# Kernel optimization log

Measured on AMD Instinct MI355X. Metric: run time of the kernel, lower is better.

Reference implementation:

```python
import jax, jax.numpy as jnp
import numpy as np

EPS = 1e-12


def _cosine_cost_volume(ref, tgt, D):
    """PSMNet-style shifted cosine-correlation cost volume, num_groups=1.
    ref, tgt: [B, C, Hf, Wf] quarter-res features. Returns [B, 1, D, Hf, Wf];
    positions w < d are 0 (zero-padded target -> zero cosine)."""
    B, C, Hf, Wf = ref.shape
    rn = ref * jax.lax.rsqrt(jnp.sum(ref * ref, axis=1, keepdims=True) + EPS)
    tn = tgt * jax.lax.rsqrt(jnp.sum(tgt * tgt, axis=1, keepdims=True) + EPS)
    pad = jnp.pad(tn, ((0, 0), (0, 0), (0, 0), (D - 1, 0)))  # left zero-pad

    def one_disp(d):
        t = jax.lax.dynamic_slice_in_dim(pad, D - 1 - d, Wf, axis=3)
        return jnp.sum(rn * t, axis=1)  # [B, Hf, Wf]

    vol = jax.vmap(one_disp)(jnp.arange(D))  # [D, B, Hf, Wf]
    return jnp.transpose(vol, (1, 0, 2, 3))[:, None]  # [B, 1, D, Hf, Wf]


def setup_inputs() -> dict:
    key = jax.random.key(0)
    k1, k2 = jax.random.split(key)
    B, C, Hf, Wf = 1, 32, 96, 192  # quarter-res ViT features (out_feats=32)
    left_fea = jax.random.normal(k1, (B, C, Hf, Wf), dtype=jnp.float32)
    right_fea = jax.random.normal(k2, (B, C, Hf, Wf), dtype=jnp.float32)
    return {"left_fea": left_fea, "right_fea": right_fea, "H": 384, "W": 768, "maxdisp": 192}


def reference(left_fea, right_fea, H, W, maxdisp):
    B = left_fea.shape[0]
    # training-branch cost volume (W//4 disparity levels, not detached in source)
    cost_init = _cosine_cost_volume(left_fea, right_fea, W // 4)
    # inference path: maxdisp//4 levels, trilinear upsample to [maxdisp, H, W]
    cost = _cosine_cost_volume(left_fea, right_fea, maxdisp // 4)
    cost = jax.lax.stop_gradient(cost)
    cost_up = jax.image.resize(cost, (B, 1, maxdisp, H, W), method="trilinear")
    pred = jnp.argmax(cost_up, axis=2)  # [B, 1, H, W]
    pred = jnp.maximum(pred, 1).astype(jnp.float32)  # pred[pred<1]=1
    return cost_init, pred
```

## Files before the change

### kernel.cpp

```cpp
#include <hip/hip_runtime.h>
#include <math.h>

#define HF 96
#define WF 192
#define CC 32
#define NPIX (HF*WF)
#define DFULL 192
#define DQ 48
#define HO 384
#define WO 768
#define SR 200

__global__ __launch_bounds__(256) void kcost(const float* __restrict__ L,
                                             const float* __restrict__ R,
                                             float* __restrict__ out) {
    __shared__ __align__(16) float Ls[CC * WF];
    __shared__ __align__(16) float Rb[CC * SR];
    const int h = blockIdx.x;
    const int tid = threadIdx.x;

    for (int i = tid; i < CC * 4; i += 256) Rb[(i >> 2) * SR + (i & 3)] = 0.0f;

    if (tid < WF) {
        const int w = tid;
        float lr[CC], rr[CC];
        float sl = 0.0f, sr = 0.0f;
        #pragma unroll
        for (int c = 0; c < CC; ++c) {
            float lv = L[c * NPIX + h * WF + w];
            float rv = R[c * NPIX + h * WF + w];
            lr[c] = lv; rr[c] = rv;
            sl = fmaf(lv, lv, sl);
            sr = fmaf(rv, rv, sr);
        }
        const float il = 1.0f / sqrtf(sl + 1e-12f);
        const float ir = 1.0f / sqrtf(sr + 1e-12f);
        #pragma unroll
        for (int c = 0; c < CC; ++c) {
            Ls[c * WF + w] = lr[c] * il;
            Rb[c * SR + 4 + w] = rr[c] * ir;
        }
    }
    __syncthreads();

    const int t = blockIdx.y * 256 + tid;
    if (t >= 1176) return;

    const int u = 1175 - t;
    int wu = (int)((sqrtf(8.0f * (float)u + 1.0f) - 1.0f) * 0.5f);
    while ((wu + 1) * (wu + 2) / 2 <= u) ++wu;
    while (wu * (wu + 1) / 2 > u) --wu;
    const int du = u - wu * (wu + 1) / 2;
    const int wt = 47 - du;
    const int dt = 47 - wu;

    const int w0 = wt * 4, d0 = dt * 4;
    const int base = w0 - d0;

    float a00=0,a01=0,a02=0,a03=0;
    float a10=0,a11=0,a12=0,a13=0;
    float a20=0,a21=0,a22=0,a23=0;
    float a30=0,a31=0,a32=0,a33=0;

    #pragma unroll 4
    for (int c = 0; c < CC; ++c) {
        const float4 lv = *(const float4*)&Ls[c * WF + w0];
        const float4 r0 = *(const float4*)&Rb[c * SR + base];
        const float4 r1 = *(const float4*)&Rb[c * SR + base + 4];
        a00 = fmaf(lv.x, r1.x, a00); a01 = fmaf(lv.y, r1.y, a01);
        a02 = fmaf(lv.z, r1.z, a02); a03 = fmaf(lv.w, r1.w, a03);
        a10 = fmaf(lv.x, r0.w, a10); a11 = fmaf(lv.y, r1.x, a11);
        a12 = fmaf(lv.z, r1.y, a12); a13 = fmaf(lv.w, r1.z, a13);
        a20 = fmaf(lv.x, r0.z, a20); a21 = fmaf(lv.y, r0.w, a21);
        a22 = fmaf(lv.z, r1.x, a22); a23 = fmaf(lv.w, r1.y, a23);
        a30 = fmaf(lv.x, r0.y, a30); a31 = fmaf(lv.y, r0.z, a31);
        a32 = fmaf(lv.z, r0.w, a32); a33 = fmaf(lv.w, r1.x, a33);
    }

    {
        float4 v;
        v.x=a00; v.y=a01; v.z=a02; v.w=a03;
        *(float4*)&out[(d0 + 0) * NPIX + h * WF + w0] = v;
        v.x=a10; v.y=a11; v.z=a12; v.w=a13;
        *(float4*)&out[(d0 + 1) * NPIX + h * WF + w0] = v;
        v.x=a20; v.y=a21; v.z=a22; v.w=a23;
        *(float4*)&out[(d0 + 2) * NPIX + h * WF + w0] = v;
        v.x=a30; v.y=a31; v.z=a32; v.w=a33;
        *(float4*)&out[(d0 + 3) * NPIX + h * WF + w0] = v;
    }

    if (wt > dt) {
        const int za = (wt - dt - 1) * 4;
        const int zb = (47 - dt) * 4;
        const float4 z = {0.0f, 0.0f, 0.0f, 0.0f};
        #pragma unroll
        for (int j = 0; j < 4; ++j)
            *(float4*)&out[(zb + j) * NPIX + h * WF + za] = z;
    }
}

__global__ __launch_bounds__(256) void kpred(const float* __restrict__ cost,
                                             float* __restrict__ pred) {
    const int mIdx = blockIdx.x * 64 + threadIdx.x;
    const int h = blockIdx.y * 4 + threadIdx.y;
    if (mIdx > 192) return;
    const int m = mIdx - 1;

    float sh = (float)(2 * h - 3) * 0.125f;
    float fh = sh - floorf(sh);
    int h0 = (int)floorf(sh);
    int h1 = h0 + 1;
    if (h0 < 0)      { h0 = 0; h1 = 0; fh = 0.0f; }
    if (h1 > HF - 1) { h1 = HF - 1;    fh = 0.0f; }
    const float wh0 = 1.0f - fh, wh1 = fh;

    const bool edge = (m < 0) || (m >= WF - 1);
    const int w0 = (m < 0) ? 0 : ((m >= WF - 1) ? WF - 1 : m);
    const int w1 = (m < 0) ? 0 : ((m >= WF - 1) ? WF - 1 : m + 1);

    float fr[4];
    #pragma unroll
    for (int r = 0; r < 4; ++r) fr[r] = edge ? 0.0f : (0.125f + 0.25f * (float)r);

    const int i00 = h0 * WF + w0;
    const int i10 = h1 * WF + w0;
    const int i01 = h0 * WF + w1;
    const int i11 = h1 * WF + w1;

    float bp[4], best[4];
    int bi[4];
    {
        const float* s = cost;
        float q00 = s[i00], q10 = s[i10], q01 = s[i01], q11 = s[i11];
        float A0 = fmaf(wh1, q10, wh0 * q00);
        float A1 = fmaf(wh1, q11, wh0 * q01);
        #pragma unroll
        for (int r = 0; r < 4; ++r) {
            bp[r] = fmaf(fr[r], A1, (1.0f - fr[r]) * A0);
            best[r] = bp[r];
            bi[r] = 0;
        }
    }

    for (int k = 1; k < DQ; ++k) {
        const float* s = cost + k * NPIX;
        float q00 = s[i00], q10 = s[i10], q01 = s[i01], q11 = s[i11];
        float A0 = fmaf(wh1, q10, wh0 * q00);
        float A1 = fmaf(wh1, q11, wh0 * q01);
        #pragma unroll
        for (int r = 0; r < 4; ++r) {
            float b = fmaf(fr[r], A1, (1.0f - fr[r]) * A0);
            float cand; int ci;
            if (b > bp[r]) { cand = fmaf(0.875f, b, 0.125f * bp[r]); ci = 4 * k + 1; }
            else           { cand = fmaf(0.125f, b, 0.875f * bp[r]); ci = 4 * k - 2; }
            if (cand > best[r]) { best[r] = cand; bi[r] = ci; }
            bp[r] = b;
        }
    }
    #pragma unroll
    for (int r = 0; r < 4; ++r)
        if (bp[r] > best[r]) bi[r] = 190;

    float v[4];
    #pragma unroll
    for (int r = 0; r < 4; ++r) v[r] = (float)(bi[r] < 1 ? 1 : bi[r]);

    float* prow = pred + h * WO;
    if (m < 0) {
        float2 o; o.x = v[0]; o.y = v[0];
        *(float2*)&prow[0] = o;
    } else if (m >= WF - 1) {
        float2 o; o.x = v[0]; o.y = v[0];
        *(float2*)&prow[WO - 2] = o;
    } else {
        float2 o0; o0.x = v[0]; o0.y = v[1];
        float2 o1; o1.x = v[2]; o1.y = v[3];
        *(float2*)&prow[4 * m + 2] = o0;
        *(float2*)&prow[4 * m + 4] = o1;
    }
}

extern "C" void kernel_launch(void* const* d_in, const int* in_sizes, int n_in,
                              void* d_out, int out_size, void* d_ws, size_t ws_size,
                              hipStream_t stream) {
    const float* L = (const float*)d_in[0];
    const float* R = (const float*)d_in[1];
    float* out = (float*)d_out;
    float* pred = out + DFULL * NPIX;

    kcost<<<dim3(HF, 5), 256, 0, stream>>>(L, R, out);
    kpred<<<dim3(4, HF), dim3(64, 4), 0, stream>>>(out, pred);
}
```

Before: 99.02 us.

## Use 4x8 register tiles and direct grid mapping in cost-volume kernel

Each thread of the cost-volume kernel now computes a 4-wide by 8-disparity tile instead of 4x4, and the triangular index decoding with sqrt and fix-up loops is replaced by a plain row-major tile index. Tiles that lie entirely in the w<d region simply write zeros and exit. Blocks shrink to 192 threads on a 96x6 grid, and the shared right-feature buffer gets an 8-element zero pad. The larger tile reuses each left-feature shared-memory load across more FMAs, at the cost of more registers and some idle threads on zero tiles.

```diff
diff --git a/kernel.cpp b/kernel.cpp
--- a/kernel.cpp
+++ b/kernel.cpp
@@ -9,19 +9,19 @@
 #define DQ 48
 #define HO 384
 #define WO 768
-#define SR 200
+#define SR2 200
 
-__global__ __launch_bounds__(256) void kcost(const float* __restrict__ L,
+__global__ __launch_bounds__(192) void kcost(const float* __restrict__ L,
                                              const float* __restrict__ R,
                                              float* __restrict__ out) {
     __shared__ __align__(16) float Ls[CC * WF];
-    __shared__ __align__(16) float Rb[CC * SR];
+    __shared__ __align__(16) float Rb[CC * SR2];
     const int h = blockIdx.x;
     const int tid = threadIdx.x;
 
-    for (int i = tid; i < CC * 4; i += 256) Rb[(i >> 2) * SR + (i & 3)] = 0.0f;
+    for (int i = tid; i < CC * 8; i += 192) Rb[(i >> 3) * SR2 + (i & 7)] = 0.0f;
 
-    if (tid < WF) {
+    {
         const int w = tid;
         float lr[CC], rr[CC];
         float sl = 0.0f, sr = 0.0f;
@@ -38,64 +38,54 @@
         #pragma unroll
         for (int c = 0; c < CC; ++c) {
             Ls[c * WF + w] = lr[c] * il;
-            Rb[c * SR + 4 + w] = rr[c] * ir;
+            Rb[c * SR2 + 8 + w] = rr[c] * ir;
         }
     }
     __syncthreads();
 
-    const int t = blockIdx.y * 256 + tid;
-    if (t >= 1176) return;
+    const int t = blockIdx.y * 192 + tid;
+    const int dt = t / 48;
+    const int wt = t - dt * 48;
+    const int w0 = wt * 4, d0 = dt * 8;
 
-    const int u = 1175 - t;
-    int wu = (int)((sqrtf(8.0f * (float)u + 1.0f) - 1.0f) * 0.5f);
-    while ((wu + 1) * (wu + 2) / 2 <= u) ++wu;
-    while (wu * (wu + 1) / 2 > u) --wu;
-    const int du = u - wu * (wu + 1) / 2;
-    const int wt = 47 - du;
-    const int dt = 47 - wu;
+    if (wt < 2 * dt) {
+        const float4 z = {0.0f, 0.0f, 0.0f, 0.0f};
+        #pragma unroll
+        for (int j = 0; j < 8; ++j)
+            *(float4*)&out[(d0 + j) * NPIX + h * WF + w0] = z;
+        return;
+    }
 
-    const int w0 = wt * 4, d0 = dt * 4;
     const int base = w0 - d0;
 
-    float a00=0,a01=0,a02=0,a03=0;
-    float a10=0,a11=0,a12=0,a13=0;
-    float a20=0,a21=0,a22=0,a23=0;
-    float a30=0,a31=0,a32=0,a33=0;
+    float acc[8][4];
+    #pragma unroll
+    for (int j = 0; j < 8; ++j)
+        #pragma unroll
+        for (int i = 0; i < 4; ++i) acc[j][i] = 0.0f;
 
     #pragma unroll 4
     for (int c = 0; c < CC; ++c) {
-        const float4 lv = *(const float4*)&Ls[c * WF + w0];
-        const float4 r0 = *(const float4*)&Rb[c * SR + base];
-        const float4 r1 = *(const float4*)&Rb[c * SR + base + 4];
-        a00 = fmaf(lv.x, r1.x, a00); a01 = fmaf(lv.y, r1.y, a01);
-        a02 = fmaf(lv.z, r1.z, a02); a03 = fmaf(lv.w, r1.w, a03);
-        a10 = fmaf(lv.x, r0.w, a10); a11 = fmaf(lv.y, r1.x, a11);
-        a12 = fmaf(lv.z, r1.y, a12); a13 = fmaf(lv.w, r1.z, a13);
-        a20 = fmaf(lv.x, r0.z, a20); a21 = fmaf(lv.y, r0.w, a21);
-        a22 = fmaf(lv.z, r1.x, a22); a23 = fmaf(lv.w, r1.y, a23);
-        a30 = fmaf(lv.x, r0.y, a30); a31 = fmaf(lv.y, r0.z, a31);
-        a32 = fmaf(lv.z, r0.w, a32); a33 = fmaf(lv.w, r1.x, a33);
+        const float4 lq = *(const float4*)&Ls[c * WF + w0];
+        const float lv[4] = {lq.x, lq.y, lq.z, lq.w};
+        float rr[12];
+        const float4 ra = *(const float4*)&Rb[c * SR2 + base];
+        const float4 rb = *(const float4*)&Rb[c * SR2 + base + 4];
+        const float4 rc = *(const float4*)&Rb[c * SR2 + base + 8];
+        rr[0]=ra.x; rr[1]=ra.y; rr[2]=ra.z; rr[3]=ra.w;
+        rr[4]=rb.x; rr[5]=rb.y; rr[6]=rb.z; rr[7]=rb.w;
+        rr[8]=rc.x; rr[9]=rc.y; rr[10]=rc.z; rr[11]=rc.w;
+        #pragma unroll
+        for (int j = 0; j < 8; ++j)
+            #pragma unroll
+            for (int i = 0; i < 4; ++i)
+                acc[j][i] = fmaf(lv[i], rr[8 + i - j], acc[j][i]);
     }
 
-    {
-        float4 v;
-        v.x=a00; v.y=a01; v.z=a02; v.w=a03;
-        *(float4*)&out[(d0 + 0) * NPIX + h * WF + w0] = v;
-        v.x=a10; v.y=a11; v.z=a12; v.w=a13;
-        *(float4*)&out[(d0 + 1) * NPIX + h * WF + w0] = v;
-        v.x=a20; v.y=a21; v.z=a22; v.w=a23;
-        *(float4*)&out[(d0 + 2) * NPIX + h * WF + w0] = v;
-        v.x=a30; v.y=a31; v.z=a32; v.w=a33;
-        *(float4*)&out[(d0 + 3) * NPIX + h * WF + w0] = v;
-    }
-
-    if (wt > dt) {
-        const int za = (wt - dt - 1) * 4;
-        const int zb = (47 - dt) * 4;
-        const float4 z = {0.0f, 0.0f, 0.0f, 0.0f};
-        #pragma unroll
-        for (int j = 0; j < 4; ++j)
-            *(float4*)&out[(zb + j) * NPIX + h * WF + za] = z;
+    #pragma unroll
+    for (int j = 0; j < 8; ++j) {
+        float4 v; v.x = acc[j][0]; v.y = acc[j][1]; v.z = acc[j][2]; v.w = acc[j][3];
+        *(float4*)&out[(d0 + j) * NPIX + h * WF + w0] = v;
     }
 }
 
@@ -188,6 +178,6 @@
     float* out = (float*)d_out;
     float* pred = out + DFULL * NPIX;
 
-    kcost<<<dim3(HF, 5), 256, 0, stream>>>(L, R, out);
+    kcost<<<dim3(HF, 6), 192, 0, stream>>>(L, R, out);
     kpred<<<dim3(4, HF), dim3(64, 4), 0, stream>>>(out, pred);
 }
```

Result: no change. 100.7 us (+1.7%).
